# Performance work log

Hardware: AMD Instinct MI355X
Metric: run time of the kernel (lower is better)

## Reference

```python
import jax, jax.numpy as jnp
import numpy as np
import math
from jax import lax

D_MODEL = 128
N_HEADS = 8
D_HEAD = D_MODEL // N_HEADS
D_FF = 4 * D_MODEL
KERNEL = 25  # moving_avg kernel size
N_LAYERS = 2
EPS = 1e-5


def moving_avg(x):
    # x: [B, L, D]; replicate-pad (KERNEL-1)//2 at both ends, window mean (AvgPool1d stride 1)
    p = (KERNEL - 1) // 2
    xp = jnp.concatenate([jnp.repeat(x[:, :1], p, axis=1), x, jnp.repeat(x[:, -1:], p, axis=1)], axis=1)
    s = lax.reduce_window(xp, 0.0, lax.add, (1, KERNEL, 1), (1, 1, 1), 'VALID')
    return s / KERNEL


def series_decomp(x):
    mm = moving_avg(x)
    return x - mm, mm


def autocorrelation(q, k, v):
    # q,k,v: [B, L, H, E]; FFT-based period correlation + top-k time-delay aggregation (training path)
    B, L, H, E = q.shape
    top_k = int(1 * math.log(L))  # factor=1
    qf = jnp.fft.rfft(q.transpose(0, 2, 3, 1), axis=-1)
    kf = jnp.fft.rfft(k.transpose(0, 2, 3, 1), axis=-1)
    corr = jnp.fft.irfft(qf * jnp.conj(kf), n=L, axis=-1)  # [B, H, E, L]
    vals = v.transpose(0, 2, 3, 1)                          # [B, H, E, L]
    mean_value = corr.mean(axis=(1, 2))                     # [B, L]
    _, index = lax.top_k(mean_value.mean(axis=0), top_k)    # [top_k], lags shared over batch
    weights = mean_value[:, index]                          # [B, top_k]
    tmp_corr = jax.nn.softmax(weights, axis=-1)
    agg = jnp.zeros_like(vals)
    for i in range(top_k):  # static small loop (top_k = 8)
        pattern = jnp.roll(vals, -index[i], axis=-1)
        agg = agg + pattern * tmp_corr[:, i][:, None, None, None]
    return agg.transpose(0, 3, 1, 2)  # [B, L, H, E]


def attn_layer(x, w, b):
    # w: [4, D, D] (q,k,v,out torch-Linear weights), b: [4, D]
    B, L, D = x.shape
    q = (jnp.einsum('bld,ed->ble', x, w[0]) + b[0]).reshape(B, L, N_HEADS, D_HEAD)
    k = (jnp.einsum('bld,ed->ble', x, w[1]) + b[1]).reshape(B, L, N_HEADS, D_HEAD)
    v = (jnp.einsum('bld,ed->ble', x, w[2]) + b[2]).reshape(B, L, N_HEADS, D_HEAD)
    o = autocorrelation(q, k, v).reshape(B, L, D)
    return jnp.einsum('bld,ed->ble', o, w[3]) + b[3]


def encoder_layer(x, w, b, w1, w2):
    x = x + attn_layer(x, w, b)
    x, _ = series_decomp(x)
    y = jax.nn.gelu(jnp.einsum('bld,fd->blf', x, w1), approximate=False)  # conv1 (k=1, no bias)
    y = jnp.einsum('blf,df->bld', y, w2)                                   # conv2 (k=1, no bias)
    res, _ = series_decomp(x + y)
    return res


def reference(x_enc, emb_w, attn_w, attn_b, ffn_w1, ffn_w2, norm_g, norm_b, fc1_w, fc1_b, fc2_w, fc2_b):
    # token embedding: Conv1d(C -> D, kernel 3, circular padding, no bias)
    xc = x_enc.transpose(0, 2, 1)  # [B, C, L]
    xc = jnp.concatenate([xc[:, :, -1:], xc, xc[:, :, :1]], axis=-1)
    h = lax.conv_general_dilated(xc, emb_w, (1,), 'VALID', dimension_numbers=('NCH', 'OIH', 'NCH'))
    h = h.transpose(0, 2, 1)  # [B, L, D]
    for l in range(N_LAYERS):
        h = encoder_layer(h, attn_w[l], attn_b[l], ffn_w1[l], ffn_w2[l])
    # my_Layernorm: LayerNorm then subtract time-mean
    mu = h.mean(axis=-1, keepdims=True)
    var = ((h - mu) ** 2).mean(axis=-1, keepdims=True)
    ln = (h - mu) / jnp.sqrt(var + EPS) * norm_g + norm_b
    h = ln - ln.mean(axis=1, keepdims=True)
    # head: gelu -> mean pool over time -> MLP
    h = jax.nn.gelu(h, approximate=False).mean(axis=1)  # [B, D]
    h = jax.nn.relu(jnp.einsum('bd,hd->bh', h, fc1_w) + fc1_b)
    return jnp.einsum('bh,ch->bc', h, fc2_w) + fc2_b


def setup_inputs() -> dict:
    key = jax.random.key(0)
    ks = jax.random.split(key, 8)
    B, L, C, NC, FC = 32, 4096, 12, 5, 128
    s = 0.02
    return {
        'x_enc': jax.random.normal(ks[0], (B, L, C), jnp.float32),
        'emb_w': jax.random.normal(ks[1], (D_MODEL, C, 3), jnp.float32) * s,
        'attn_w': jax.random.normal(ks[2], (N_LAYERS, 4, D_MODEL, D_MODEL), jnp.float32) * s,
        'attn_b': jnp.zeros((N_LAYERS, 4, D_MODEL), jnp.float32),
        'ffn_w1': jax.random.normal(ks[3], (N_LAYERS, D_FF, D_MODEL), jnp.float32) * s,
        'ffn_w2': jax.random.normal(ks[4], (N_LAYERS, D_MODEL, D_FF), jnp.float32) * s,
        'norm_g': jnp.ones((D_MODEL,), jnp.float32),
        'norm_b': jnp.zeros((D_MODEL,), jnp.float32),
        'fc1_w': jax.random.normal(ks[5], (FC, D_MODEL), jnp.float32) * s,
        'fc1_b': jnp.zeros((FC,), jnp.float32),
        'fc2_w': jax.random.normal(ks[6], (NC, FC), jnp.float32) * s,
        'fc2_b': jnp.zeros((NC,), jnp.float32),
    }
```

## Files before the change

kernel.cpp:

```cpp
#include <hip/hip_runtime.h>
#include <math.h>

#define L_SEQ 4096
#define BATCH 32
#define DM 128

typedef short short8 __attribute__((ext_vector_type(8)));
typedef float f32x4 __attribute__((ext_vector_type(4)));

__device__ __forceinline__ float gelu_f(float x) {
    return 0.5f * x * (1.0f + erff(x * 0.70710678118654752f));
}
__device__ __forceinline__ float gelu_fast(float x) {
    float ax = fabsf(x);
    if (ax < 1.0f) {
        float z = x * 0.70710678118654752f;
        float z2 = z * z;
        float p = 1.0f + z2 * (-0.333333333f + z2 * (0.1f + z2 * (-0.0238095238f +
                  z2 * (4.62962963e-3f + z2 * (-7.57575758e-4f)))));
        return 0.5f * x * (1.0f + 1.1283791670955126f * z * p);
    }
    return 0.5f * x * (1.0f + erff(x * 0.70710678118654752f));
}
__device__ __forceinline__ unsigned short f2b(float f) {
    unsigned u = __float_as_uint(f);
    u += 0x7fffu + ((u >> 16) & 1u);
    return (unsigned short)(u >> 16);
}
__device__ __forceinline__ float b2f(unsigned short h) {
    return __uint_as_float(((unsigned)h) << 16);
}

__global__ __launch_bounds__(256) void kembed(const float* __restrict__ x,
                                              const float* __restrict__ w,
                                              float* __restrict__ h) {
    __shared__ float xs[130][12];
    __shared__ float wsm[128][37];
    int b = blockIdx.x >> 5;
    int lt = blockIdx.x & 31;
    int l0 = lt * 128;
    int tid = threadIdx.x;
    for (int i = tid; i < 130 * 12; i += 256) {
        int r = i / 12, c = i - r * 12;
        int gl = (l0 - 1 + r + 4096) & 4095;
        xs[r][c] = x[((size_t)b * 4096 + gl) * 12 + c];
    }
    for (int i = tid; i < 128 * 36; i += 256) {
        int o = i / 36, j = i - o * 36;
        wsm[o][j] = w[i];
    }
    __syncthreads();
    int o = tid & 127, lh = tid >> 7;
    float wr[36];
#pragma unroll
    for (int j = 0; j < 36; j++) wr[j] = wsm[o][j];
    int base_r = lh * 64;
    float ring[4][12];
#pragma unroll
    for (int c = 0; c < 12; c++) { ring[0][c] = xs[base_r][c]; ring[1][c] = xs[base_r + 1][c]; }
    float* hp = h + ((size_t)b * 4096 + l0 + lh * 64) * 128 + o;
#pragma unroll 4
    for (int st = 0; st < 64; st++) {
        int s0 = st & 3, s1 = (st + 1) & 3, s2 = (st + 2) & 3;
#pragma unroll
        for (int c = 0; c < 12; c++) ring[s2][c] = xs[base_r + st + 2][c];
        float s = 0.f;
#pragma unroll
        for (int c = 0; c < 12; c++)
            s += wr[c * 3 + 0] * ring[s0][c] + wr[c * 3 + 1] * ring[s1][c] + wr[c * 3 + 2] * ring[s2][c];
        hp[(size_t)st * 128] = s;
    }
}

__global__ __launch_bounds__(256) void kprepw(const float* __restrict__ w1,
                                              const float* __restrict__ w2,
                                              const float* __restrict__ attn_w,
                                              unsigned short* __restrict__ w1img,
                                              unsigned short* __restrict__ w2img,
                                              unsigned short* __restrict__ qkh,
                                              unsigned short* __restrict__ qkl,
                                              unsigned short* __restrict__ voimg) {
    int t = blockIdx.x * 256 + threadIdx.x;
    if (t < 262144) {
        int layer = t >> 17; int rem = t & 131071;
        if (rem < 65536) {
            int R = rem >> 7, x = rem & 127;
            int g = x >> 3, j = x & 7;
            int srcc = ((g ^ (R & 7)) << 3) + j;
            w1img[(size_t)layer * 65536 + rem] = f2b(w1[(size_t)layer * 65536 + R * 128 + srcc]);
        } else {
            int r2 = rem - 65536;
            int c = r2 >> 13; int D = (r2 >> 6) & 127; int x = r2 & 63;
            int g = x >> 3, j = x & 7;
            int srcf = c * 64 + ((g ^ (D & 7)) << 3) + j;
            w2img[(size_t)layer * 65536 + r2] = f2b(w2[(size_t)layer * 65536 + D * 512 + srcf]);
        }
    } else if (t < 327680) {
        int t2 = t - 262144;
        int layer = t2 >> 15; int rem = t2 & 32767;
        int y = rem >> 14; int rem2 = rem & 16383;
        int r64 = rem2 >> 7; int x = rem2 & 127;
        int r = r64 & 63;
        int g = x >> 3, j = x & 7;
        int srcc = ((g ^ (r & 7)) << 3) + j;
        float v = attn_w[(size_t)layer * 65536 + y * 16384 + r64 * 128 + srcc];
        unsigned short hh = f2b(v);
        qkh[t2] = hh;
        qkl[t2] = f2b(v - b2f(hh));
    } else {
        int t3 = t - 327680;
        int layer = t3 >> 15; int rem = t3 & 32767;
        int mat = rem >> 14; int rem2 = rem & 16383;
        int r = rem2 >> 7; int x = rem2 & 127;
        int g = x >> 3, j = x & 7;
        int srcc = ((g ^ (r & 7)) << 3) + j;
        voimg[t3] = f2b(attn_w[(size_t)layer * 65536 + (2 + mat) * 16384 + r * 128 + srcc]);
    }
}

__global__ __launch_bounds__(256, 2) void kgemm_qk3(const float* __restrict__ A,
                                                    const unsigned short* __restrict__ qkh,
                                                    const unsigned short* __restrict__ qkl,
                                                    const float* __restrict__ ab,
                                                    int half, float* __restrict__ CT) {
    __shared__ __align__(16) char smem[65536];
    short* Ah = (short*)smem;
    short* Al = (short*)(smem + 16384);
    short* Wh = (short*)(smem + 32768);
    short* Wl = (short*)(smem + 49152);
    int y = blockIdx.y;
    const unsigned short* wh = qkh + y * 16384 + half * 8192;
    const unsigned short* wl = qkl + y * 16384 + half * 8192;
    const float* bias = ab + y * 128 + half * 64;
    int row0 = blockIdx.x * 64;
    int tid = threadIdx.x;
#pragma unroll
    for (int u = 0; u < 4; u++) {
        int task = tid + u * 256;
        int r = task >> 4, cg = task & 15;
        int dst = r * 128 + ((cg ^ (r & 7)) << 3);
        const float* src = A + ((size_t)(row0 + r)) * 128 + cg * 8;
        float4 xa = *(const float4*)src, ya = *(const float4*)(src + 4);
        float av[8] = {xa.x, xa.y, xa.z, xa.w, ya.x, ya.y, ya.z, ya.w};
        short8 hi, lo;
#pragma unroll
        for (int j = 0; j < 8; j++) {
            unsigned short h = f2b(av[j]);
            hi[j] = (short)h; lo[j] = (short)f2b(av[j] - b2f(h));
        }
        *(short8*)(Ah + dst) = hi; *(short8*)(Al + dst) = lo;
        int lin = r * 128 + cg * 8;
        *(short8*)(Wh + lin) = *(const short8*)(wh + lin);
        *(short8*)(Wl + lin) = *(const short8*)(wl + lin);
    }
    __syncthreads();
    int l = tid & 63; int w = tid >> 6; int wm = w >> 1, wn = w & 1;
    f32x4 acc[2][2];
#pragma unroll
    for (int i = 0; i < 2; i++)
#pragma unroll
        for (int j = 0; j < 2; j++) acc[i][j] = (f32x4){0.f, 0.f, 0.f, 0.f};
#pragma unroll
    for (int ks = 0; ks < 4; ks++) {
        int cg = ks * 4 + (l >> 4);
        short8 ah[2], al2[2], bh[2], bl[2];
#pragma unroll
        for (int mi = 0; mi < 2; mi++) {
            int rm = wm * 32 + mi * 16 + (l & 15);
            int off = rm * 128 + ((cg ^ (rm & 7)) << 3);
            ah[mi] = *(short8*)(Ah + off); al2[mi] = *(short8*)(Al + off);
        }
#pragma unroll
        for (int ni = 0; ni < 2; ni++) {
            int rn = wn * 32 + ni * 16 + (l & 15);
            int off = rn * 128 + ((cg ^ (rn & 7)) << 3);
            bh[ni] = *(short8*)(Wh + off); bl[ni] = *(short8*)(Wl + off);
        }
#pragma unroll
        for (int mi = 0; mi < 2; mi++)
#pragma unroll
            for (int ni = 0; ni < 2; ni++) {
                acc[mi][ni] = __builtin_amdgcn_mfma_f32_16x16x32_bf16(ah[mi], bh[ni], acc[mi][ni], 0, 0, 0);
                acc[mi][ni] = __builtin_amdgcn_mfma_f32_16x16x32_bf16(ah[mi], bl[ni], acc[mi][ni], 0, 0, 0);
                acc[mi][ni] = __builtin_amdgcn_mfma_f32_16x16x32_bf16(al2[mi], bh[ni], acc[mi][ni], 0, 0, 0);
            }
    }
    __syncthreads();
    float* Dsh = (float*)smem;
#pragma unroll
    for (int mi = 0; mi < 2; mi++)
#pragma unroll
        for (int ni = 0; ni < 2; ni++)
#pragma unroll
            for (int rr = 0; rr < 4; rr++) {
                int m = wm * 32 + mi * 16 + (l >> 4) * 4 + rr;
                int n = wn * 32 + ni * 16 + (l & 15);
                Dsh[n * 68 + m] = acc[mi][ni][rr] + bias[n];
            }
    __syncthreads();
    int b = row0 >> 12; int l0 = row0 & 4095;
    int cbase = y * 64;
#pragma unroll
    for (int u = 0; u < 4; u++) {
        int task = tid + u * 256;
        int c = task >> 4, m4 = (task & 15) * 4;
        float4 v = *(float4*)&Dsh[c * 68 + m4];
        *(float4*)&CT[((size_t)(b * 128 + cbase + c)) * 4096 + l0 + m4] = v;
    }
}

template <int AT, int EPI>
__global__ __launch_bounds__(256, 2) void kgemm_mfma(const void* __restrict__ Ap,
                                                     const unsigned short* __restrict__ Wimg,
                                                     const float* __restrict__ bias,
                                                     const float* __restrict__ res,
                                                     const float* __restrict__ tcb,
                                                     const int* __restrict__ idxb,
                                                     void* __restrict__ outp) {
    __shared__ __align__(16) char smem[65536];
    short* As = (short*)smem;
    short* Ws = (short*)(smem + 32768);
    int tid = threadIdx.x;
    size_t row0 = (size_t)blockIdx.x * 128;
#pragma unroll
    for (int u = 0; u < 8; u++) {
        int g = tid + u * 256;
        int r = g >> 4, cg = g & 15;
        int dsti = r * 128 + ((cg ^ (r & 7)) << 3);
        short8 v;
        if (AT == 0) {
            const float* src = (const float*)Ap + (row0 + r) * 128 + cg * 8;
            float4 x = *(const float4*)src, y = *(const float4*)(src + 4);
            v[0] = f2b(x.x); v[1] = f2b(x.y); v[2] = f2b(x.z); v[3] = f2b(x.w);
            v[4] = f2b(y.x); v[5] = f2b(y.y); v[6] = f2b(y.z); v[7] = f2b(y.w);
        } else {
            const unsigned short* Vb = (const unsigned short*)Ap;
            int b = (int)(row0 >> 12);
            int l0 = (int)(row0 & 4095);
            float accv[8];
#pragma unroll
            for (int j = 0; j < 8; j++) accv[j] = 0.f;
#pragma unroll
            for (int i = 0; i < 8; i++) {
                float wgt = tcb[b * 8 + i];
                int lr = (l0 + r + idxb[i]) & 4095;
                short8 vv = *(const short8*)(Vb + ((size_t)(b * 4096 + lr)) * 128 + cg * 8);
#pragma unroll
                for (int j = 0; j < 8; j++) accv[j] += wgt * b2f((unsigned short)vv[j]);
            }
#pragma unroll
            for (int j = 0; j < 8; j++) v[j] = (short)f2b(accv[j]);
        }
        *(short8*)(As + dsti) = v;
        int lin = r * 128 + cg * 8;
        *(short8*)(Ws + lin) = *(const short8*)(Wimg + lin);
    }
    __syncthreads();
    int l = tid & 63; int w = tid >> 6; int wm = w >> 1, wn = w & 1;
    f32x4 acc[4][4];
#pragma unroll
    for (int i = 0; i < 4; i++)
#pragma unroll
        for (int j = 0; j < 4; j++) acc[i][j] = (f32x4){0.f, 0.f, 0.f, 0.f};
#pragma unroll
    for (int ks = 0; ks < 4; ks++) {
        int cg = ks * 4 + (l >> 4);
        short8 af[4], bf[4];
#pragma unroll
        for (int mi = 0; mi < 4; mi++) {
            int rm = wm * 64 + mi * 16 + (l & 15);
            af[mi] = *(short8*)(As + rm * 128 + ((cg ^ (rm & 7)) << 3));
        }
#pragma unroll
        for (int ni = 0; ni < 4; ni++) {
            int rn = wn * 64 + ni * 16 + (l & 15);
            bf[ni] = *(short8*)(Ws + rn * 128 + ((cg ^ (rn & 7)) << 3));
        }
#pragma unroll
        for (int mi = 0; mi < 4; mi++)
#pragma unroll
            for (int ni = 0; ni < 4; ni++)
                acc[mi][ni] = __builtin_amdgcn_mfma_f32_16x16x32_bf16(af[mi], bf[ni], acc[mi][ni], 0, 0, 0);
    }
    __syncthreads();
    float* Dsh = (float*)smem;
#pragma unroll
    for (int mi = 0; mi < 4; mi++)
#pragma unroll
        for (int ni = 0; ni < 4; ni++)
#pragma unroll
            for (int rr = 0; rr < 4; rr++)
                Dsh[(wm * 64 + mi * 16 + (l >> 4) * 4 + rr) * 128 + wn * 64 + ni * 16 + (l & 15)] = acc[mi][ni][rr];
    __syncthreads();
#pragma unroll
    for (int u = 0; u < 8; u++) {
        int g = tid + u * 256;
        int r = g >> 4, c8 = (g & 15) * 8;
        float vv[8];
#pragma unroll
        for (int j = 0; j < 8; j++) vv[j] = Dsh[r * 128 + c8 + j] + bias[c8 + j];
        if (EPI == 1) {
            const float* rp = res + (row0 + r) * 128 + c8;
#pragma unroll
            for (int j = 0; j < 8; j++) vv[j] += rp[j];
            float* op = (float*)outp + (row0 + r) * 128 + c8;
            *(float4*)op = make_float4(vv[0], vv[1], vv[2], vv[3]);
            *(float4*)(op + 4) = make_float4(vv[4], vv[5], vv[6], vv[7]);
        } else {
            short8 ov;
#pragma unroll
            for (int j = 0; j < 8; j++) ov[j] = (short)f2b(vv[j]);
            *(short8*)((short*)outp + (row0 + r) * 128 + c8) = ov;
        }
    }
}

__global__ __launch_bounds__(256, 2) void kffn_mfma(const float* __restrict__ xs,
                                                    const unsigned short* __restrict__ w1img,
                                                    const unsigned short* __restrict__ w2img,
                                                    float* __restrict__ outp) {
    __shared__ __align__(16) char smem[81920];
    short* xsl = (short*)smem;
    short* w1t = (short*)(smem + 32768);
    short* tt  = (short*)(smem + 49152);
    short* w2t = (short*)(smem + 65536);
    int tid = threadIdx.x;
    size_t row0 = (size_t)blockIdx.x * 128;
#pragma unroll
    for (int u = 0; u < 8; u++) {
        int g = tid + u * 256;
        int r = g >> 4, cg = g & 15;
        const float* src = xs + (row0 + r) * 128 + cg * 8;
        float4 x = *(const float4*)src, y = *(const float4*)(src + 4);
        short8 v;
        v[0] = f2b(x.x); v[1] = f2b(x.y); v[2] = f2b(x.z); v[3] = f2b(x.w);
        v[4] = f2b(y.x); v[5] = f2b(y.y); v[6] = f2b(y.z); v[7] = f2b(y.w);
        *(short8*)(xsl + r * 128 + ((cg ^ (r & 7)) << 3)) = v;
    }
    int l = tid & 63; int w = tid >> 6; int wm = w >> 1, wn = w & 1;
    f32x4 acc2[4][4];
#pragma unroll
    for (int i = 0; i < 4; i++)
#pragma unroll
        for (int j = 0; j < 4; j++) acc2[i][j] = (f32x4){0.f, 0.f, 0.f, 0.f};
    for (int fb = 0; fb < 8; fb++) {
        __syncthreads();
#pragma unroll
        for (int u = 0; u < 4; u++) {
            int task = tid + u * 256;
            int r = task >> 4, cg = task & 15;
            *(short8*)(w1t + r * 128 + cg * 8) =
                *(const short8*)(w1img + ((size_t)(fb * 64 + r)) * 128 + cg * 8);
            int r2 = task >> 3, cg2 = task & 7;
            *(short8*)(w2t + r2 * 64 + cg2 * 8) =
                *(const short8*)(w2img + ((size_t)(fb * 128 + r2)) * 64 + cg2 * 8);
        }
        __syncthreads();
        f32x4 a1[4][2];
#pragma unroll
        for (int i = 0; i < 4; i++)
#pragma unroll
            for (int j = 0; j < 2; j++) a1[i][j] = (f32x4){0.f, 0.f, 0.f, 0.f};
#pragma unroll
        for (int ks = 0; ks < 4; ks++) {
            int cg = ks * 4 + (l >> 4);
            short8 af[4], bf[2];
#pragma unroll
            for (int mi = 0; mi < 4; mi++) {
                int rm = wm * 64 + mi * 16 + (l & 15);
                af[mi] = *(short8*)(xsl + rm * 128 + ((cg ^ (rm & 7)) << 3));
            }
#pragma unroll
            for (int ni = 0; ni < 2; ni++) {
                int rn = wn * 32 + ni * 16 + (l & 15);
                bf[ni] = *(short8*)(w1t + rn * 128 + ((cg ^ (rn & 7)) << 3));
            }
#pragma unroll
            for (int mi = 0; mi < 4; mi++)
#pragma unroll
                for (int ni = 0; ni < 2; ni++)
                    a1[mi][ni] = __builtin_amdgcn_mfma_f32_16x16x32_bf16(af[mi], bf[ni], a1[mi][ni], 0, 0, 0);
        }
#pragma unroll
        for (int mi = 0; mi < 4; mi++)
#pragma unroll
            for (int ni = 0; ni < 2; ni++)
#pragma unroll
                for (int rr = 0; rr < 4; rr++) {
                    int m = wm * 64 + mi * 16 + (l >> 4) * 4 + rr;
                    int f = wn * 32 + ni * 16 + (l & 15);
                    tt[m * 64 + (((f >> 3) ^ (m & 7)) << 3) + (f & 7)] = (short)f2b(gelu_fast(a1[mi][ni][rr]));
                }
        __syncthreads();
#pragma unroll
        for (int ks = 0; ks < 2; ks++) {
            int cg = ks * 4 + (l >> 4);
            short8 af[4], bf[4];
#pragma unroll
            for (int mi = 0; mi < 4; mi++) {
                int rm = wm * 64 + mi * 16 + (l & 15);
                af[mi] = *(short8*)(tt + rm * 64 + ((cg ^ (rm & 7)) << 3));
            }
#pragma unroll
            for (int ni = 0; ni < 4; ni++) {
                int rn = wn * 64 + ni * 16 + (l & 15);
                bf[ni] = *(short8*)(w2t + rn * 64 + ((cg ^ (rn & 7)) << 3));
            }
#pragma unroll
            for (int mi = 0; mi < 4; mi++)
#pragma unroll
                for (int ni = 0; ni < 4; ni++)
                    acc2[mi][ni] = __builtin_amdgcn_mfma_f32_16x16x32_bf16(af[mi], bf[ni], acc2[mi][ni], 0, 0, 0);
        }
    }
    __syncthreads();
    float* Dsh = (float*)smem;
#pragma unroll
    for (int mi = 0; mi < 4; mi++)
#pragma unroll
        for (int ni = 0; ni < 4; ni++)
#pragma unroll
            for (int rr = 0; rr < 4; rr++)
                Dsh[(wm * 64 + mi * 16 + (l >> 4) * 4 + rr) * 128 + wn * 64 + ni * 16 + (l & 15)] = acc2[mi][ni][rr];
    __syncthreads();
#pragma unroll
    for (int u = 0; u < 8; u++) {
        int g = tid + u * 256;
        int r = g >> 4, c8 = (g & 15) * 8;
        const float* rp = xs + (row0 + r) * 128 + c8;
        float* op = outp + (row0 + r) * 128 + c8;
        float4 o0, o1;
        o0.x = Dsh[r * 128 + c8 + 0] + rp[0]; o0.y = Dsh[r * 128 + c8 + 1] + rp[1];
        o0.z = Dsh[r * 128 + c8 + 2] + rp[2]; o0.w = Dsh[r * 128 + c8 + 3] + rp[3];
        o1.x = Dsh[r * 128 + c8 + 4] + rp[4]; o1.y = Dsh[r * 128 + c8 + 5] + rp[5];
        o1.z = Dsh[r * 128 + c8 + 6] + rp[6]; o1.w = Dsh[r * 128 + c8 + 7] + rp[7];
        *(float4*)op = o0; *(float4*)(op + 4) = o1;
    }
}

#define FIDX(a) ((a) + ((a) >> 4))

__device__ __forceinline__ float2 twget(const float2* __restrict__ tw, int a, float sgn) {
    float2 T = tw[a & 1023];
    int hi = (a >> 10) & 3;
    float cs = (hi & 1) ? ((hi & 2) ? T.y : -T.y) : ((hi & 2) ? -T.x : T.x);
    float sn = (hi & 1) ? ((hi & 2) ? -T.x : T.x) : ((hi & 2) ? -T.y : T.y);
    return make_float2(cs, sn * sgn);
}

__device__ void fft4096_r4(float2* __restrict__ b0, float2* __restrict__ b1,
                           const float2* __restrict__ tw, float sgn, int tid) {
    float2* cur = b0; float2* nxt = b1;
#pragma unroll
    for (int t = 0; t < 6; t++) {
        int s = 1 << (t << 1);
        int q = tid & (s - 1);
        int ps = tid - q;
        float2 a0 = cur[FIDX(tid)];
        float2 a1 = cur[FIDX(tid + 1024)];
        float2 a2 = cur[FIDX(tid + 2048)];
        float2 a3 = cur[FIDX(tid + 3072)];
        float t0x = a0.x + a2.x, t0y = a0.y + a2.y;
        float t1x = a0.x - a2.x, t1y = a0.y - a2.y;
        float t2x = a1.x + a3.x, t2y = a1.y + a3.y;
        float t3x = a1.x - a3.x, t3y = a1.y - a3.y;
        float it3x = -sgn * t3y, it3y = sgn * t3x;
        float2 A0 = make_float2(t0x + t2x, t0y + t2y);
        float2 A1 = make_float2(t1x + it3x, t1y + it3y);
        float2 A2 = make_float2(t0x - t2x, t0y - t2y);
        float2 A3 = make_float2(t1x - it3x, t1y - it3y);
        int ob = q + (ps << 2);
        nxt[FIDX(ob)] = A0;
        float2 w1 = twget(tw, ps, sgn);
        float2 w2 = twget(tw, ps * 2, sgn);
        float2 w3 = twget(tw, ps * 3, sgn);
        nxt[FIDX(ob + s)] = make_float2(A1.x * w1.x - A1.y * w1.y, A1.x * w1.y + A1.y * w1.x);
        nxt[FIDX(ob + 2 * s)] = make_float2(A2.x * w2.x - A2.y * w2.y, A2.x * w2.y + A2.y * w2.x);
        nxt[FIDX(ob + 3 * s)] = make_float2(A3.x * w3.x - A3.y * w3.y, A3.x * w3.y + A3.y * w3.x);
        __syncthreads();
        float2* tp = cur; cur = nxt; nxt = tp;
    }
}

__global__ __launch_bounds__(1024) void kfft_fwd(const float* __restrict__ qkT,
                                                 float* __restrict__ Pws, int ghalf) {
    __shared__ float2 bufA[4352];
    __shared__ float2 bufB[4352];
    __shared__ float2 tw[1024];
    int tid = threadIdx.x;
    {
        float sn, cs;
        sincosf(1.5339807878856412e-3f * (float)tid, &sn, &cs);
        tw[tid] = make_float2(cs, sn);
    }
    int b = blockIdx.x >> 4;
    int g = blockIdx.x & 15;
    float2 pacc[4];
#pragma unroll
    for (int j = 0; j < 4; j++) pacc[j] = make_float2(0.f, 0.f);
    for (int c4 = 0; c4 < 4; c4++) {
        int c = g * 4 + c4;
        const float* qrow = qkT + ((size_t)(b * 128 + c)) * 4096;
        const float* krow = qkT + ((size_t)(b * 128 + 64 + c)) * 4096;
        __syncthreads();
        int i0 = tid * 4;
        float4 qv = *(const float4*)(qrow + i0);
        float4 kv = *(const float4*)(krow + i0);
        bufA[FIDX(i0)]     = make_float2(qv.x, kv.x);
        bufA[FIDX(i0 + 1)] = make_float2(qv.y, kv.y);
        bufA[FIDX(i0 + 2)] = make_float2(qv.z, kv.z);
        bufA[FIDX(i0 + 3)] = make_float2(qv.w, kv.w);
        __syncthreads();
        fft4096_r4(bufA, bufB, tw, -1.f, tid);
#pragma unroll
        for (int j = 0; j < 4; j++) {
            int f = tid + j * 1024;
            float2 Zf = bufA[FIDX(f)];
            float2 Zm = bufA[FIDX((4096 - f) & 4095)];
            float Qre = 0.5f * (Zf.x + Zm.x), Qim = 0.5f * (Zf.y - Zm.y);
            float Kre = 0.5f * (Zf.y + Zm.y), Kim = -0.5f * (Zf.x - Zm.x);
            pacc[j].x += Qre * Kre + Qim * Kim;
            pacc[j].y += Qim * Kre - Qre * Kim;
        }
    }
    float2* P = (float2*)Pws + (size_t)(b * 16 + g) * 4096;
    if (ghalf == 0) {
#pragma unroll
        for (int j = 0; j < 4; j++) { int f = tid + j * 1024; P[f] = pacc[j]; }
    } else {
#pragma unroll
        for (int j = 0; j < 4; j++) {
            int f = tid + j * 1024;
            float2 r = P[f];
            P[f] = make_float2(r.x + pacc[j].x, r.y + pacc[j].y);
        }
    }
}

__global__ __launch_bounds__(1024) void kfft_inv(const float* __restrict__ Pws,
                                                 float* __restrict__ meanv) {
    __shared__ float2 bufA[4352];
    __shared__ float2 bufB[4352];
    __shared__ float2 tw[1024];
    int tid = threadIdx.x;
    {
        float sn, cs;
        sincosf(1.5339807878856412e-3f * (float)tid, &sn, &cs);
        tw[tid] = make_float2(cs, sn);
    }
    int b = blockIdx.x;
    const float2* P = (const float2*)Pws + (size_t)b * 16 * 4096;
#pragma unroll
    for (int j = 0; j < 4; j++) {
        int i = tid + j * 1024;
        float2 s = make_float2(0.f, 0.f);
#pragma unroll
        for (int gg = 0; gg < 16; gg++) { float2 v = P[gg * 4096 + i]; s.x += v.x; s.y += v.y; }
        bufA[FIDX(i)] = s;
    }
    __syncthreads();
    fft4096_r4(bufA, bufB, tw, 1.f, tid);
    const float scale = 1.0f / (4096.0f * 128.0f);
#pragma unroll
    for (int j = 0; j < 4; j++) {
        int i = tid + j * 1024;
        meanv[b * 4096 + i] = bufA[FIDX(i)].x * scale;
    }
}

__global__ __launch_bounds__(256) void kcolsum(const float* __restrict__ meanv,
                                               float* __restrict__ cmg) {
    int c = blockIdx.x * 256 + threadIdx.x;
    float s = 0.f;
    for (int b = 0; b < 32; b++) s += meanv[b * 4096 + c];
    cmg[c] = s;
}

__global__ __launch_bounds__(256) void ktopk2(const float* __restrict__ cmg,
                                              const float* __restrict__ meanv,
                                              int* __restrict__ idxout,
                                              float* __restrict__ tc) {
    __shared__ float cm[4096];
    __shared__ float rv[256];
    __shared__ int ri[256];
    __shared__ int sidx[8];
    for (int c = threadIdx.x; c < 4096; c += 256) cm[c] = cmg[c];
    __syncthreads();
    for (int it = 0; it < 8; it++) {
        float bv = -1e30f; int bi = 0;
        for (int c = threadIdx.x; c < 4096; c += 256) {
            float v = cm[c];
            if (v > bv) { bv = v; bi = c; }
        }
        rv[threadIdx.x] = bv; ri[threadIdx.x] = bi;
        __syncthreads();
        for (int off = 128; off > 0; off >>= 1) {
            if (threadIdx.x < off) {
                float v2 = rv[threadIdx.x + off]; int i2 = ri[threadIdx.x + off];
                if (v2 > rv[threadIdx.x] || (v2 == rv[threadIdx.x] && i2 < ri[threadIdx.x])) {
                    rv[threadIdx.x] = v2; ri[threadIdx.x] = i2;
                }
            }
            __syncthreads();
        }
        if (threadIdx.x == 0) { sidx[it] = ri[0]; idxout[it] = ri[0]; cm[ri[0]] = -1e30f; }
        __syncthreads();
    }
    if (threadIdx.x < 32) {
        int b = threadIdx.x;
        float w[8]; float mx = -1e30f;
#pragma unroll
        for (int i = 0; i < 8; i++) { w[i] = meanv[b * 4096 + sidx[i]]; mx = fmaxf(mx, w[i]); }
        float s = 0.f;
#pragma unroll
        for (int i = 0; i < 8; i++) { w[i] = expf(w[i] - mx); s += w[i]; }
#pragma unroll
        for (int i = 0; i < 8; i++) tc[b * 8 + i] = w[i] / s;
    }
}

__global__ __launch_bounds__(256) void kdecomp(const float* __restrict__ in,
                                               float* __restrict__ outp) {
    int b = blockIdx.x >> 4; int lc = blockIdx.x & 15;
    int dg = threadIdx.x & 31; int ls = threadIdx.x >> 5;
    int l0 = lc * 256 + ls * 32;
    const float* base = in + (size_t)b * 524288 + dg * 4;
    float* ob = outp + (size_t)b * 524288 + dg * 4;
    float sx = 0.f, sy = 0.f, sz = 0.f, sw = 0.f;
#pragma unroll
    for (int j = -12; j <= 12; j++) {
        int lj = l0 + j;
        lj = lj < 0 ? 0 : (lj > 4095 ? 4095 : lj);
        float4 v = *(const float4*)(base + (size_t)lj * 128);
        sx += v.x; sy += v.y; sz += v.z; sw += v.w;
    }
    for (int st = 0; st < 32; st++) {
        int l = l0 + st;
        float4 c = *(const float4*)(base + (size_t)l * 128);
        float4 o = make_float4(c.x - sx * (1.0f / 25.0f), c.y - sy * (1.0f / 25.0f),
                               c.z - sz * (1.0f / 25.0f), c.w - sw * (1.0f / 25.0f));
        *(float4*)(ob + (size_t)l * 128) = o;
        int ln = l + 13 > 4095 ? 4095 : l + 13;
        int lo2 = l - 12 < 0 ? 0 : l - 12;
        float4 vn = *(const float4*)(base + (size_t)ln * 128);
        float4 vo = *(const float4*)(base + (size_t)lo2 * 128);
        sx += vn.x - vo.x; sy += vn.y - vo.y; sz += vn.z - vo.z; sw += vn.w - vo.w;
    }
}

__global__ __launch_bounds__(256) void kln_part1(float* __restrict__ h,
                                                 const float* __restrict__ g,
                                                 const float* __restrict__ bb,
                                                 float* __restrict__ part) {
    __shared__ float sh[4][128];
    int b = blockIdx.x >> 5;
    int sl = blockIdx.x & 31;
    int w = threadIdx.x >> 6;
    int lane = threadIdx.x & 63;
    float2 gv = *(const float2*)(g + lane * 2);
    float2 bv = *(const float2*)(bb + lane * 2);
    size_t r0 = (size_t)b * 4096 + sl * 128 + w * 32;
    float c0 = 0.f, c1 = 0.f;
    for (int i = 0; i < 32; i++) {
        float* p = h + (r0 + i) * 128 + lane * 2;
        float2 v = *(float2*)p;
        float s = v.x + v.y, s2 = v.x * v.x + v.y * v.y;
#pragma unroll
        for (int off = 32; off; off >>= 1) { s += __shfl_down(s, off); s2 += __shfl_down(s2, off); }
        s = __shfl(s, 0); s2 = __shfl(s2, 0);
        float mu = s * (1.f / 128.f);
        float var = s2 * (1.f / 128.f) - mu * mu;
        float inv = rsqrtf(var + 1e-5f);
        float o0 = (v.x - mu) * inv * gv.x + bv.x;
        float o1 = (v.y - mu) * inv * gv.y + bv.y;
        *(float2*)p = make_float2(o0, o1);
        c0 += o0; c1 += o1;
    }
    sh[w][lane * 2] = c0; sh[w][lane * 2 + 1] = c1;
    __syncthreads();
    if (threadIdx.x < 128) {
        int d = threadIdx.x;
        part[(size_t)(b * 32 + sl) * 128 + d] = sh[0][d] + sh[1][d] + sh[2][d] + sh[3][d];
    }
}

__global__ __launch_bounds__(128) void kpart2(const float* __restrict__ part,
                                              float* __restrict__ outm, int nq) {
    int b = blockIdx.x; int d = threadIdx.x;
    float s = 0.f;
    for (int q = 0; q < nq; q++) s += part[(size_t)(b * nq + q) * 128 + d];
    outm[b * 128 + d] = s * (1.f / 4096.f);
}

__global__ __launch_bounds__(256) void kgpart1(const float* __restrict__ h,
                                               const float* __restrict__ msum,
                                               float* __restrict__ part) {
    int b = blockIdx.x >> 3, sl = blockIdx.x & 7;
    int d = threadIdx.x & 127, p = threadIdx.x >> 7;
    const float* base = h + ((size_t)b * 4096 + sl * 512) * 128;
    float m = msum[b * 128 + d];
    float acc = 0.f;
    for (int l = p; l < 512; l += 2) acc += gelu_f(base[(size_t)l * 128 + d] - m);
    __shared__ float sh[256];
    sh[threadIdx.x] = acc; __syncthreads();
    if (p == 0) part[(size_t)(b * 8 + sl) * 128 + d] = acc + sh[128 + d];
}

__global__ __launch_bounds__(256) void khead(const float* __restrict__ gmean,
                                             const float* __restrict__ fc1w,
                                             const float* __restrict__ fc1b,
                                             const float* __restrict__ fc2w,
                                             const float* __restrict__ fc2b,
                                             float* __restrict__ outp) {
    __shared__ float h0[32][128];
    __shared__ float h1[32][128];
    int tid = threadIdx.x;
#pragma unroll
    for (int i = 0; i < 16; i++) {
        int e = tid + i * 256;
        h0[e >> 7][e & 127] = gmean[e];
    }
    __syncthreads();
#pragma unroll
    for (int i = 0; i < 16; i++) {
        int e = tid + i * 256; int b = e >> 7, j = e & 127;
        float s = fc1b[j];
        for (int d = 0; d < 128; d++) s += h0[b][d] * fc1w[j * 128 + d];
        h1[b][j] = fmaxf(s, 0.f);
    }
    __syncthreads();
    if (tid < 160) {
        int b = tid / 5, c2 = tid % 5;
        float s = fc2b[c2];
        for (int j = 0; j < 128; j++) s += h1[b][j] * fc2w[c2 * 128 + j];
        outp[b * 5 + c2] = s;
    }
}

extern "C" void kernel_launch(void* const* d_in, const int* in_sizes, int n_in,
                              void* d_out, int out_size, void* d_ws, size_t ws_size,
                              hipStream_t stream) {
    const float* x_enc  = (const float*)d_in[0];
    const float* emb_w  = (const float*)d_in[1];
    const float* attn_w = (const float*)d_in[2];
    const float* attn_b = (const float*)d_in[3];
    const float* ffn_w1 = (const float*)d_in[4];
    const float* ffn_w2 = (const float*)d_in[5];
    const float* norm_g = (const float*)d_in[6];
    const float* norm_b = (const float*)d_in[7];
    const float* fc1_w  = (const float*)d_in[8];
    const float* fc1_b  = (const float*)d_in[9];
    const float* fc2_w  = (const float*)d_in[10];
    const float* fc2_b  = (const float*)d_in[11];
    float* outp = (float*)d_out;

    float* W = (float*)d_ws;
    const size_t RD = (size_t)BATCH * L_SEQ * DM;
    float* buf0  = W;
    float* buf1  = W + RD;
    float* Pws   = W + 2 * RD;
    float* meanv = Pws + (size_t)4194304;
    float* tcb   = meanv + (size_t)131072;
    int*   idxb  = (int*)(tcb + 256);
    float* part  = tcb + 256 + 64;
    float* msum  = part + 32768;
    float* gsum  = msum + 4096;
    unsigned short* w1img = (unsigned short*)(gsum + 4096);
    unsigned short* w2img = w1img + (size_t)2 * 65536;
    unsigned short* qkh   = w2img + (size_t)2 * 65536;
    unsigned short* qkl   = qkh + (size_t)65536;
    unsigned short* voimg = qkl + (size_t)65536;
    float* cmg   = (float*)(voimg + (size_t)65536);

    kembed<<<1024, 256, 0, stream>>>(x_enc, emb_w, buf0);
    kprepw<<<1536, 256, 0, stream>>>(ffn_w1, ffn_w2, attn_w, w1img, w2img, qkh, qkl, voimg);

    float* H = buf0;
    float* S = buf1;
    for (int l = 0; l < 2; l++) {
        const float* ab = attn_b + (size_t)l * 4 * 128;
        for (int half = 0; half < 2; half++) {
            kgemm_qk3<<<dim3(2048, 2), 256, 0, stream>>>(H, qkh + (size_t)l * 32768,
                                                         qkl + (size_t)l * 32768, ab, half, S);
            kfft_fwd<<<512, 1024, 0, stream>>>(S, Pws, half);
        }
        kfft_inv<<<32, 1024, 0, stream>>>(Pws, meanv);
        kcolsum<<<16, 256, 0, stream>>>(meanv, cmg);
        ktopk2<<<1, 256, 0, stream>>>(cmg, meanv, idxb, tcb);
        unsigned short* Vb = (unsigned short*)S;
        kgemm_mfma<0, 0><<<1024, 256, 0, stream>>>(H, voimg + (size_t)l * 32768, ab + 256,
                                                   nullptr, nullptr, nullptr, Vb);
        kgemm_mfma<2, 1><<<1024, 256, 0, stream>>>(Vb, voimg + (size_t)l * 32768 + 16384, ab + 384,
                                                   H, tcb, idxb, H);
        kdecomp<<<512, 256, 0, stream>>>(H, S);
        kffn_mfma<<<1024, 256, 0, stream>>>(S, w1img + (size_t)l * 65536,
                                            w2img + (size_t)l * 65536, H);
        kdecomp<<<512, 256, 0, stream>>>(H, S);
        float* t = H; H = S; S = t;
    }

    kln_part1<<<1024, 256, 0, stream>>>(H, norm_g, norm_b, meanv);
    kpart2<<<32, 128, 0, stream>>>(meanv, msum, 32);
    kgpart1<<<256, 256, 0, stream>>>(H, msum, part);
    kpart2<<<32, 128, 0, stream>>>(part, gsum, 8);
    khead<<<1, 256, 0, stream>>>(gsum, fc1_w, fc1_b, fc2_w, fc2_b, outp);
}
```

Baseline: 1.058 ms.

## Store transposed Q/K as bf16 in one pass and prefetch FFN weights

The Q/K projection now runs as a single launch covering both halves and writes its transposed output in bf16 instead of fp32. The forward FFT then reads all 8 channels per group in one launch, and the read-modify-write accumulation into the workspace is gone. This halves the intermediate traffic and removes two launches per layer. The FFN kernel also register-prefetches the next weight tile while computing the current one. The cost is bf16 rounding of the Q/K inputs to the correlation, which can change which top-k lags are selected.

```diff
diff --git a/kernel.cpp b/kernel.cpp
--- a/kernel.cpp
+++ b/kernel.cpp
@@ -6,6 +6,7 @@
 #define DM 128
 
 typedef short short8 __attribute__((ext_vector_type(8)));
+typedef short short4v __attribute__((ext_vector_type(4)));
 typedef float f32x4 __attribute__((ext_vector_type(4)));
 
 __device__ __forceinline__ float gelu_f(float x) {
@@ -118,21 +119,22 @@
     }
 }
 
-__global__ __launch_bounds__(256, 2) void kgemm_qk3(const float* __restrict__ A,
+__global__ __launch_bounds__(256, 2) void kgemm_qkb(const float* __restrict__ A,
                                                     const unsigned short* __restrict__ qkh,
                                                     const unsigned short* __restrict__ qkl,
                                                     const float* __restrict__ ab,
-                                                    int half, float* __restrict__ CT) {
+                                                    unsigned short* __restrict__ CTb) {
     __shared__ __align__(16) char smem[65536];
     short* Ah = (short*)smem;
     short* Al = (short*)(smem + 16384);
     short* Wh = (short*)(smem + 32768);
     short* Wl = (short*)(smem + 49152);
-    int y = blockIdx.y;
+    int role = blockIdx.x;
+    int y = role >> 1, half = role & 1;
     const unsigned short* wh = qkh + y * 16384 + half * 8192;
     const unsigned short* wl = qkl + y * 16384 + half * 8192;
     const float* bias = ab + y * 128 + half * 64;
-    int row0 = blockIdx.x * 64;
+    int row0 = blockIdx.y * 64;
     int tid = threadIdx.x;
 #pragma unroll
     for (int u = 0; u < 4; u++) {
@@ -199,13 +201,16 @@
             }
     __syncthreads();
     int b = row0 >> 12; int l0 = row0 & 4095;
-    int cbase = y * 64;
+    int cb = y * 128 + half * 64;
 #pragma unroll
     for (int u = 0; u < 4; u++) {
         int task = tid + u * 256;
         int c = task >> 4, m4 = (task & 15) * 4;
         float4 v = *(float4*)&Dsh[c * 68 + m4];
-        *(float4*)&CT[((size_t)(b * 128 + cbase + c)) * 4096 + l0 + m4] = v;
+        short4v o;
+        o[0] = (short)f2b(v.x); o[1] = (short)f2b(v.y);
+        o[2] = (short)f2b(v.z); o[3] = (short)f2b(v.w);
+        *(short4v*)&CTb[((size_t)(b * 256 + cb + c)) * 4096 + l0 + m4] = o;
     }
 }
 
@@ -315,6 +320,17 @@
     }
 }
 
+#define LOADW(FB) do { \
+    _Pragma("unroll") \
+    for (int u = 0; u < 4; u++) { \
+        int task = tid + u * 256; \
+        int r = task >> 4, cg = task & 15; \
+        p1[u] = *(const short8*)(w1img + ((size_t)((FB) * 64 + r)) * 128 + cg * 8); \
+        int r2 = task >> 3, cg2 = task & 7; \
+        p2[u] = *(const short8*)(w2img + ((size_t)((FB) * 128 + r2)) * 64 + cg2 * 8); \
+    } \
+} while (0)
+
 __global__ __launch_bounds__(256, 2) void kffn_mfma(const float* __restrict__ xs,
                                                     const unsigned short* __restrict__ w1img,
                                                     const unsigned short* __restrict__ w2img,
@@ -343,19 +359,20 @@
     for (int i = 0; i < 4; i++)
 #pragma unroll
         for (int j = 0; j < 4; j++) acc2[i][j] = (f32x4){0.f, 0.f, 0.f, 0.f};
+    short8 p1[4], p2[4];
+    LOADW(0);
     for (int fb = 0; fb < 8; fb++) {
         __syncthreads();
 #pragma unroll
         for (int u = 0; u < 4; u++) {
             int task = tid + u * 256;
             int r = task >> 4, cg = task & 15;
-            *(short8*)(w1t + r * 128 + cg * 8) =
-                *(const short8*)(w1img + ((size_t)(fb * 64 + r)) * 128 + cg * 8);
+            *(short8*)(w1t + r * 128 + cg * 8) = p1[u];
             int r2 = task >> 3, cg2 = task & 7;
-            *(short8*)(w2t + r2 * 64 + cg2 * 8) =
-                *(const short8*)(w2img + ((size_t)(fb * 128 + r2)) * 64 + cg2 * 8);
+            *(short8*)(w2t + r2 * 64 + cg2 * 8) = p2[u];
         }
         __syncthreads();
+        if (fb < 7) LOADW(fb + 1);
         f32x4 a1[4][2];
 #pragma unroll
         for (int i = 0; i < 4; i++)
@@ -482,8 +499,8 @@
     }
 }
 
-__global__ __launch_bounds__(1024) void kfft_fwd(const float* __restrict__ qkT,
-                                                 float* __restrict__ Pws, int ghalf) {
+__global__ __launch_bounds__(1024) void kfft_fwd(const unsigned short* __restrict__ qkT,
+                                                 float* __restrict__ Pws) {
     __shared__ float2 bufA[4352];
     __shared__ float2 bufB[4352];
     __shared__ float2 tw[1024];
@@ -498,18 +515,18 @@
     float2 pacc[4];
 #pragma unroll
     for (int j = 0; j < 4; j++) pacc[j] = make_float2(0.f, 0.f);
-    for (int c4 = 0; c4 < 4; c4++) {
-        int c = g * 4 + c4;
-        const float* qrow = qkT + ((size_t)(b * 128 + c)) * 4096;
-        const float* krow = qkT + ((size_t)(b * 128 + 64 + c)) * 4096;
+    for (int c8 = 0; c8 < 8; c8++) {
+        int c = g * 8 + c8;
+        const unsigned short* qrow = qkT + ((size_t)(b * 256 + c)) * 4096;
+        const unsigned short* krow = qkT + ((size_t)(b * 256 + 128 + c)) * 4096;
         __syncthreads();
         int i0 = tid * 4;
-        float4 qv = *(const float4*)(qrow + i0);
-        float4 kv = *(const float4*)(krow + i0);
-        bufA[FIDX(i0)]     = make_float2(qv.x, kv.x);
-        bufA[FIDX(i0 + 1)] = make_float2(qv.y, kv.y);
-        bufA[FIDX(i0 + 2)] = make_float2(qv.z, kv.z);
-        bufA[FIDX(i0 + 3)] = make_float2(qv.w, kv.w);
+        short4v qv = *(const short4v*)(qrow + i0);
+        short4v kv = *(const short4v*)(krow + i0);
+        bufA[FIDX(i0)]     = make_float2(b2f((unsigned short)qv[0]), b2f((unsigned short)kv[0]));
+        bufA[FIDX(i0 + 1)] = make_float2(b2f((unsigned short)qv[1]), b2f((unsigned short)kv[1]));
+        bufA[FIDX(i0 + 2)] = make_float2(b2f((unsigned short)qv[2]), b2f((unsigned short)kv[2]));
+        bufA[FIDX(i0 + 3)] = make_float2(b2f((unsigned short)qv[3]), b2f((unsigned short)kv[3]));
         __syncthreads();
         fft4096_r4(bufA, bufB, tw, -1.f, tid);
 #pragma unroll
@@ -524,17 +541,8 @@
         }
     }
     float2* P = (float2*)Pws + (size_t)(b * 16 + g) * 4096;
-    if (ghalf == 0) {
-#pragma unroll
-        for (int j = 0; j < 4; j++) { int f = tid + j * 1024; P[f] = pacc[j]; }
-    } else {
-#pragma unroll
-        for (int j = 0; j < 4; j++) {
-            int f = tid + j * 1024;
-            float2 r = P[f];
-            P[f] = make_float2(r.x + pacc[j].x, r.y + pacc[j].y);
-        }
-    }
+#pragma unroll
+    for (int j = 0; j < 4; j++) { int f = tid + j * 1024; P[f] = pacc[j]; }
 }
 
 __global__ __launch_bounds__(1024) void kfft_inv(const float* __restrict__ Pws,
@@ -779,11 +787,10 @@
     float* S = buf1;
     for (int l = 0; l < 2; l++) {
         const float* ab = attn_b + (size_t)l * 4 * 128;
-        for (int half = 0; half < 2; half++) {
-            kgemm_qk3<<<dim3(2048, 2), 256, 0, stream>>>(H, qkh + (size_t)l * 32768,
-                                                         qkl + (size_t)l * 32768, ab, half, S);
-            kfft_fwd<<<512, 1024, 0, stream>>>(S, Pws, half);
-        }
+        unsigned short* CTb = (unsigned short*)S;
+        kgemm_qkb<<<dim3(4, 2048), 256, 0, stream>>>(H, qkh + (size_t)l * 32768,
+                                                     qkl + (size_t)l * 32768, ab, CTb);
+        kfft_fwd<<<512, 1024, 0, stream>>>(CTb, Pws);
         kfft_inv<<<32, 1024, 0, stream>>>(Pws, meanv);
         kcolsum<<<16, 256, 0, stream>>>(meanv, cmg);
         ktopk2<<<1, 256, 0, stream>>>(cmg, meanv, idxb, tcb);
```

Measured after the change: 1.010 ms. 4.6% less time.
